# Performance work log

Measured on AMD Instinct MI355X. Metric: run time of the kernel, lower is better.

The kernel has to match this reference:

```python
import jax, jax.numpy as jnp
import numpy as np

DIM = 2048
DIM_HEAD = 128
HEADS = 16
BATCH = 1
SEQ = 2048
EPS = 1e-5
MASK_VALUE = 1e-10  # faithful to original module (not -inf)
SCALE = DIM_HEAD ** -0.5


def setup_inputs() -> dict:
    key = jax.random.key(0)
    ks = jax.random.split(key, 7)
    x = jax.random.normal(ks[0], (BATCH, SEQ, DIM), dtype=jnp.float32)
    pos_bias = jax.random.normal(ks[1], (HEADS, SEQ, SEQ), dtype=jnp.float32)
    gamma = jnp.ones((DIM,), dtype=jnp.float32)
    wq = jax.random.normal(ks[2], (DIM, HEADS * DIM_HEAD), dtype=jnp.float32)
    wk = jax.random.normal(ks[3], (DIM, DIM_HEAD), dtype=jnp.float32)
    wv = jax.random.normal(ks[4], (DIM, DIM_HEAD), dtype=jnp.float32)
    wo = jax.random.normal(ks[5], (HEADS * DIM_HEAD, DIM), dtype=jnp.float32)
    # causal mask [SEQ, SEQ]
    mask = jnp.tril(jnp.ones((SEQ, SEQ), dtype=jnp.bool_))
    return {"x": x, "pos_bias": pos_bias, "gamma": gamma,
            "wq": wq, "wk": wk, "wv": wv, "wo": wo, "mask": mask}


def reference(x, pos_bias, gamma, wq, wk, wv, wo, mask):
    # RMSNorm
    inv_norm = jax.lax.rsqrt(jnp.mean(jnp.square(x), axis=-1, keepdims=True) + EPS)
    xn = inv_norm * x * gamma
    # projections (multi-query: single shared K/V head)
    q = xn @ wq                                  # [b, n, h*d]
    k = xn @ wk                                  # [b, n, d]
    v = xn @ wv                                  # [b, n, d]
    b, n, _ = q.shape
    q = q.reshape(b, n, HEADS, DIM_HEAD).transpose(0, 2, 1, 3)  # [b, h, n, d]
    q = q * SCALE
    sim = jnp.einsum('bhid,bjd->bhij', q, k)     # [b, h, i, j]
    sim = sim + pos_bias                          # pos_bias [h, n, n] broadcasts
    sim = jnp.where(mask, sim, MASK_VALUE)
    attn = jax.nn.softmax(sim, axis=-1)
    out = jnp.einsum('bhij,bjd->bhid', attn, v)  # [b, h, n, d]
    out = out.transpose(0, 2, 1, 3).reshape(b, n, HEADS * DIM_HEAD)
    return out @ wo
```

## Files before the change

### kernel.cpp

```cpp
#include <hip/hip_runtime.h>
#include <math.h>

#define SEQ 2048
#define DIM 2048
#define NH 16
#define DH 128
#define NKV 2304
#define KOFF 2048
#define VOFF 2176
#define QK_SCALE 0.08838834764831845f

typedef _Float16 f16;
typedef _Float16 f16x8 __attribute__((ext_vector_type(8)));
typedef _Float16 f16x4 __attribute__((ext_vector_type(4)));
typedef float f32x4 __attribute__((ext_vector_type(4)));

__global__ __launch_bounds__(256) void rmsnorm_split_k(
    const float* __restrict__ x, const float* __restrict__ gamma,
    f16* __restrict__ oh, f16* __restrict__ ol)
{
    int row = blockIdx.x, tid = threadIdx.x;
    const float4* xr = (const float4*)(x + (size_t)row * DIM);
    float4 a0 = xr[tid], a1 = xr[tid + 256];
    float ss = a0.x*a0.x + a0.y*a0.y + a0.z*a0.z + a0.w*a0.w
             + a1.x*a1.x + a1.y*a1.y + a1.z*a1.z + a1.w*a1.w;
    #pragma unroll
    for (int off = 1; off < 64; off <<= 1) ss += __shfl_xor(ss, off, 64);
    __shared__ float red[4];
    if ((tid & 63) == 0) red[tid >> 6] = ss;
    __syncthreads();
    float inv = 1.0f / sqrtf((red[0] + red[1] + red[2] + red[3]) * (1.0f / DIM) + 1e-5f);
    const float4* gr = (const float4*)gamma;
    float4 g0 = gr[tid], g1 = gr[tid + 256];
    float v[8] = { a0.x*inv*g0.x, a0.y*inv*g0.y, a0.z*inv*g0.z, a0.w*inv*g0.w,
                   a1.x*inv*g1.x, a1.y*inv*g1.y, a1.z*inv*g1.z, a1.w*inv*g1.w };
    f16x4 h0, l0, h1, l1;
    #pragma unroll
    for (int i = 0; i < 4; i++) {
        f16 h = (f16)v[i];   h0[i] = h; l0[i] = (f16)(v[i]   - (float)h);
        f16 g = (f16)v[i+4]; h1[i] = g; l1[i] = (f16)(v[i+4] - (float)g);
    }
    size_t base = (size_t)row * DIM + tid * 4;
    *(f16x4*)&oh[base] = h0;  *(f16x4*)&oh[base + 1024] = h1;
    *(f16x4*)&ol[base] = l0;  *(f16x4*)&ol[base + 1024] = l1;
}

template<bool WLO>
__global__ __launch_bounds__(256) void transpose_split_k(
    const float* __restrict__ in, f16* __restrict__ oh, f16* __restrict__ ol,
    int ldin, int outld)
{
    __shared__ float t[32][33];
    int tx = threadIdx.x, ty = threadIdx.y;
    int c0 = blockIdx.x * 32, r0 = blockIdx.y * 32;
    #pragma unroll
    for (int yy = 0; yy < 4; yy++)
        t[ty + yy*8][tx] = in[(size_t)(r0 + ty + yy*8) * ldin + c0 + tx];
    __syncthreads();
    #pragma unroll
    for (int yy = 0; yy < 4; yy++) {
        float v = t[tx][ty + yy*8];
        size_t o = (size_t)(c0 + ty + yy*8) * outld + r0 + tx;
        f16 h = (f16)v; oh[o] = h;
        if (WLO) ol[o] = (f16)(v - (float)h);
    }
}

__global__ __launch_bounds__(256) void transpose_f16_k(
    const f16* __restrict__ in, f16* __restrict__ out, int ldin, int outld)
{
    __shared__ f16 t[32][33];
    int tx = threadIdx.x, ty = threadIdx.y;
    int c0 = blockIdx.x * 32, r0 = blockIdx.y * 32;
    #pragma unroll
    for (int yy = 0; yy < 4; yy++)
        t[ty + yy*8][tx] = in[(size_t)(r0 + ty + yy*8) * ldin + c0 + tx];
    __syncthreads();
    #pragma unroll
    for (int yy = 0; yy < 4; yy++)
        out[(size_t)(c0 + ty + yy*8) * outld + r0 + tx] = t[tx][ty + yy*8];
}

template<int PASSES, int OUTMODE>
__global__ __launch_bounds__(256) void gemm_k(
    const f16* __restrict__ Ah, const f16* __restrict__ Al,
    const f16* __restrict__ Bh, const f16* __restrict__ Bl,
    float* __restrict__ C, f16* __restrict__ Ch, f16* __restrict__ Cl,
    int N, int K, float scale, int scale_cols)
{
    __shared__ f16 sa_h[128][40];
    __shared__ f16 sb_h[128][40];
    __shared__ f16 sa_l[PASSES == 3 ? 128 : 1][40];
    __shared__ f16 sb_l[PASSES == 3 ? 128 : 1][40];
    int tid = threadIdx.x;
    int wave = tid >> 6, lane = tid & 63, quad = lane >> 4, l16 = lane & 15;
    int m0 = blockIdx.x * 128, n0 = blockIdx.y * 128;
    int wm = (wave & 1) * 64, wn = (wave >> 1) * 64;
    int srow = tid >> 2, sch = (tid & 3) * 8;
    f32x4 acc[4][4] = {};
    const f16* pa0 = Ah + (size_t)(m0 + srow) * K + sch;
    const f16* pa1 = Ah + (size_t)(m0 + srow + 64) * K + sch;
    const f16* pb0 = Bh + (size_t)(n0 + srow) * K + sch;
    const f16* pb1 = Bh + (size_t)(n0 + srow + 64) * K + sch;
    const f16* qa0 = Al + (size_t)(m0 + srow) * K + sch;
    const f16* qa1 = Al + (size_t)(m0 + srow + 64) * K + sch;
    const f16* qb0 = Bl + (size_t)(n0 + srow) * K + sch;
    const f16* qb1 = Bl + (size_t)(n0 + srow + 64) * K + sch;

    for (int k0 = 0; k0 < K; k0 += 32) {
        __syncthreads();
        *(f16x8*)&sa_h[srow][sch]      = *(const f16x8*)(pa0 + k0);
        *(f16x8*)&sa_h[srow + 64][sch] = *(const f16x8*)(pa1 + k0);
        *(f16x8*)&sb_h[srow][sch]      = *(const f16x8*)(pb0 + k0);
        *(f16x8*)&sb_h[srow + 64][sch] = *(const f16x8*)(pb1 + k0);
        if constexpr (PASSES == 3) {
            *(f16x8*)&sa_l[srow][sch]      = *(const f16x8*)(qa0 + k0);
            *(f16x8*)&sa_l[srow + 64][sch] = *(const f16x8*)(qa1 + k0);
            *(f16x8*)&sb_l[srow][sch]      = *(const f16x8*)(qb0 + k0);
            *(f16x8*)&sb_l[srow + 64][sch] = *(const f16x8*)(qb1 + k0);
        }
        __syncthreads();
        f16x8 ah[4], bh[4], al[4], bl[4];
        #pragma unroll
        for (int t = 0; t < 4; t++) {
            ah[t] = *(const f16x8*)&sa_h[wm + t*16 + l16][quad * 8];
            bh[t] = *(const f16x8*)&sb_h[wn + t*16 + l16][quad * 8];
        }
        if constexpr (PASSES == 3) {
            #pragma unroll
            for (int t = 0; t < 4; t++) {
                al[t] = *(const f16x8*)&sa_l[wm + t*16 + l16][quad * 8];
                bl[t] = *(const f16x8*)&sb_l[wn + t*16 + l16][quad * 8];
            }
        }
        #pragma unroll
        for (int i = 0; i < 4; i++)
            #pragma unroll
            for (int j = 0; j < 4; j++) {
                acc[i][j] = __builtin_amdgcn_mfma_f32_16x16x32_f16(ah[i], bh[j], acc[i][j], 0, 0, 0);
                if constexpr (PASSES == 3) {
                    acc[i][j] = __builtin_amdgcn_mfma_f32_16x16x32_f16(ah[i], bl[j], acc[i][j], 0, 0, 0);
                    acc[i][j] = __builtin_amdgcn_mfma_f32_16x16x32_f16(al[i], bh[j], acc[i][j], 0, 0, 0);
                }
            }
    }
    #pragma unroll
    for (int i = 0; i < 4; i++)
        #pragma unroll
        for (int j = 0; j < 4; j++) {
            int row = m0 + wm + i*16 + quad*4;
            int col = n0 + wn + j*16 + l16;
            float s = (col < scale_cols) ? scale : 1.0f;
            #pragma unroll
            for (int r = 0; r < 4; r++) {
                float v = acc[i][j][r] * s;
                if constexpr (OUTMODE == 0) {
                    C[(size_t)(row + r) * N + col] = v;
                } else {
                    f16 h = (f16)v;
                    Ch[(size_t)(row + r) * N + col] = h;
                    Cl[(size_t)(row + r) * N + col] = (f16)(v - (float)h);
                }
            }
        }
}

__global__ __launch_bounds__(256) void attn_k(
    const f16* __restrict__ Ph, const f16* __restrict__ Pl,
    const f16* __restrict__ Vt, const float* __restrict__ bias,
    f16* __restrict__ Out)
{
    __shared__ f16 skh[64][136];
    __shared__ f16 skl[64][136];
    __shared__ f16 sv[128][72];
    __shared__ f16 sp[4][16][72];
    int tid = threadIdx.x, wave = tid >> 6, lane = tid & 63;
    int quad = lane >> 4, l16 = lane & 15;
    int h = blockIdx.y;
    int i0 = blockIdx.x * 64;
    int qrow = i0 + wave * 16 + l16;

    f16x8 qh[4], ql[4];
    #pragma unroll
    for (int kt = 0; kt < 4; kt++) {
        size_t off = (size_t)qrow * NKV + h * DH + kt * 32 + quad * 8;
        qh[kt] = *(const f16x8*)(Ph + off);
        ql[kt] = *(const f16x8*)(Pl + off);
    }
    f32x4 o[8];
    f32x4 zero = {0.f, 0.f, 0.f, 0.f};
    #pragma unroll
    for (int dt = 0; dt < 8; dt++) o[dt] = zero;
    float mrun[4], lrun[4];
    #pragma unroll
    for (int r = 0; r < 4; r++) { mrun[r] = -1e30f; lrun[r] = 0.f; }

    int krow = tid >> 2, kc4 = tid & 3;
    int vd = tid >> 1, vcg = tid & 1;
    const float* brow = bias + (size_t)h * SEQ * SEQ;
    int ibase = i0 + wave * 16 + quad * 4;

    for (int j0 = 0; j0 < SEQ; j0 += 64) {
        __syncthreads();
        #pragma unroll
        for (int cc = 0; cc < 4; cc++) {
            int ch = kc4 + cc * 4;
            size_t goff = (size_t)(j0 + krow) * NKV + KOFF + ch * 8;
            *(f16x8*)&skh[krow][ch * 8] = *(const f16x8*)(Ph + goff);
            *(f16x8*)&skl[krow][ch * 8] = *(const f16x8*)(Pl + goff);
        }
        #pragma unroll
        for (int cc = 0; cc < 4; cc++) {
            int ch = vcg + cc * 2;
            *(f16x8*)&sv[vd][ch * 8] = *(const f16x8*)(Vt + (size_t)vd * SEQ + j0 + ch * 8);
        }
        __syncthreads();

        f32x4 s[4];
        #pragma unroll
        for (int nt = 0; nt < 4; nt++) s[nt] = zero;
        #pragma unroll
        for (int nt = 0; nt < 4; nt++)
            #pragma unroll
            for (int kt = 0; kt < 4; kt++) {
                f16x8 kh = *(const f16x8*)&skh[nt*16 + l16][kt*32 + quad*8];
                f16x8 kl = *(const f16x8*)&skl[nt*16 + l16][kt*32 + quad*8];
                s[nt] = __builtin_amdgcn_mfma_f32_16x16x32_f16(qh[kt], kh, s[nt], 0, 0, 0);
                s[nt] = __builtin_amdgcn_mfma_f32_16x16x32_f16(qh[kt], kl, s[nt], 0, 0, 0);
                s[nt] = __builtin_amdgcn_mfma_f32_16x16x32_f16(ql[kt], kh, s[nt], 0, 0, 0);
            }
        #pragma unroll
        for (int nt = 0; nt < 4; nt++) {
            int jg = j0 + nt*16 + l16;
            #pragma unroll
            for (int r = 0; r < 4; r++) {
                int ig = ibase + r;
                float v = s[nt][r] + brow[(size_t)ig * SEQ + jg];
                s[nt][r] = (jg <= ig) ? v : 1e-10f;
            }
        }
        #pragma unroll
        for (int r = 0; r < 4; r++) {
            float mx = fmaxf(fmaxf(s[0][r], s[1][r]), fmaxf(s[2][r], s[3][r]));
            mx = fmaxf(mx, __shfl_xor(mx, 1, 64));
            mx = fmaxf(mx, __shfl_xor(mx, 2, 64));
            mx = fmaxf(mx, __shfl_xor(mx, 4, 64));
            mx = fmaxf(mx, __shfl_xor(mx, 8, 64));
            float mn = fmaxf(mrun[r], mx);
            float alpha = __expf(mrun[r] - mn);
            mrun[r] = mn;
            float rs = 0.f;
            #pragma unroll
            for (int nt = 0; nt < 4; nt++) {
                float p = __expf(s[nt][r] - mn);
                s[nt][r] = p; rs += p;
            }
            rs += __shfl_xor(rs, 1, 64);
            rs += __shfl_xor(rs, 2, 64);
            rs += __shfl_xor(rs, 4, 64);
            rs += __shfl_xor(rs, 8, 64);
            lrun[r] = lrun[r] * alpha + rs;
            #pragma unroll
            for (int dt = 0; dt < 8; dt++) o[dt][r] *= alpha;
            #pragma unroll
            for (int nt = 0; nt < 4; nt++)
                sp[wave][quad*4 + r][nt*16 + l16] = (f16)s[nt][r];
        }
        #pragma unroll
        for (int ks = 0; ks < 2; ks++) {
            f16x8 pa = *(const f16x8*)&sp[wave][l16][ks*32 + quad*8];
            #pragma unroll
            for (int dt = 0; dt < 8; dt++) {
                f16x8 vb = *(const f16x8*)&sv[dt*16 + l16][ks*32 + quad*8];
                o[dt] = __builtin_amdgcn_mfma_f32_16x16x32_f16(pa, vb, o[dt], 0, 0, 0);
            }
        }
    }
    #pragma unroll
    for (int dt = 0; dt < 8; dt++) {
        int col = h * DH + dt*16 + l16;
        #pragma unroll
        for (int r = 0; r < 4; r++) {
            int ig = i0 + wave*16 + quad*4 + r;
            Out[(size_t)ig * DIM + col] = (f16)(o[dt][r] / lrun[r]);
        }
    }
}

extern "C" void kernel_launch(void* const* d_in, const int* in_sizes, int n_in,
                              void* d_out, int out_size, void* d_ws, size_t ws_size,
                              hipStream_t stream)
{
    const float* x     = (const float*)d_in[0];
    const float* bias  = (const float*)d_in[1];
    const float* gamma = (const float*)d_in[2];
    const float* wq    = (const float*)d_in[3];
    const float* wk    = (const float*)d_in[4];
    const float* wv    = (const float*)d_in[5];
    const float* wo    = (const float*)d_in[6];
    float* out = (float*)d_out;
    char* ws = (char*)d_ws;

    const size_t MB = 1024 * 1024;
    f16* xn_h   = (f16*)(ws);
    f16* xn_l   = (f16*)(ws + 8  * MB);
    f16* wT_h   = (f16*)(ws + 16 * MB);
    f16* wT_l   = (f16*)(ws + 25 * MB);
    f16* woT_h  = (f16*)(ws + 34 * MB);
    f16* proj_h = (f16*)(ws + 42 * MB);
    f16* proj_l = (f16*)(ws + 51 * MB);
    f16* attn_o = xn_h;
    f16* vT     = xn_l;

    dim3 tb(32, 8);

    rmsnorm_split_k<<<SEQ, 256, 0, stream>>>(x, gamma, xn_h, xn_l);

    transpose_split_k<true><<<dim3(64, 64), tb, 0, stream>>>(wq, wT_h, wT_l, DIM, DIM);
    transpose_split_k<true><<<dim3(4, 64),  tb, 0, stream>>>(wk, wT_h + (size_t)KOFF * DIM,
                                                             wT_l + (size_t)KOFF * DIM, DH, DIM);
    transpose_split_k<true><<<dim3(4, 64),  tb, 0, stream>>>(wv, wT_h + (size_t)VOFF * DIM,
                                                             wT_l + (size_t)VOFF * DIM, DH, DIM);
    transpose_split_k<false><<<dim3(64, 64), tb, 0, stream>>>(wo, woT_h, nullptr, DIM, DIM);

    gemm_k<3, 1><<<dim3(16, 18), 256, 0, stream>>>(xn_h, xn_l, wT_h, wT_l,
                                                   nullptr, proj_h, proj_l,
                                                   NKV, DIM, QK_SCALE, DIM);

    transpose_f16_k<<<dim3(4, 64), tb, 0, stream>>>(proj_h + VOFF, vT, NKV, SEQ);

    attn_k<<<dim3(32, 16), 256, 0, stream>>>(proj_h, proj_l, vT, bias, attn_o);

    gemm_k<1, 0><<<dim3(16, 16), 256, 0, stream>>>(attn_o, attn_o, woT_h, woT_h,
                                                   out, nullptr, nullptr,
                                                   DIM, DIM, 1.0f, 0);
}
```

Before: 642.7 us.

## Skip masked attention tiles via closed-form suffix sum; use direct global-to-LDS loads in GEMM

The attention kernel now iterates only over key tiles up to the causal diagonal. A precomputed suffix sum of V accounts in closed form for the masked positions, which carry the constant logit 1e-10, so their contribution is folded into the final softmax normalization exactly. Query blocks are launched in reverse order so the longest blocks start first. The GEMM replaces register-staged shared-memory stores with global_load_lds into unpadded tiles, which may add LDS bank conflicts in exchange for lower register and VALU cost.

```diff
diff --git a/kernel.cpp b/kernel.cpp
--- a/kernel.cpp
+++ b/kernel.cpp
@@ -14,6 +14,13 @@
 typedef _Float16 f16x8 __attribute__((ext_vector_type(8)));
 typedef _Float16 f16x4 __attribute__((ext_vector_type(4)));
 typedef float f32x4 __attribute__((ext_vector_type(4)));
+
+__device__ __forceinline__ void gload16(const f16* g, f16* l) {
+    __builtin_amdgcn_global_load_lds(
+        (const __attribute__((address_space(1))) void*)g,
+        (__attribute__((address_space(3))) void*)l,
+        16, 0, 0);
+}
 
 __global__ __launch_bounds__(256) void rmsnorm_split_k(
     const float* __restrict__ x, const float* __restrict__ gamma,
@@ -81,6 +88,28 @@
         out[(size_t)(c0 + ty + yy*8) * outld + r0 + tx] = t[tx][ty + yy*8];
 }
 
+__global__ __launch_bounds__(64) void vsuf_k(
+    const f16* __restrict__ Vt, float* __restrict__ Vsuf)
+{
+    int d = blockIdx.x;
+    int lane = threadIdx.x;
+    float vals[32]; float s = 0.f;
+    const f16* row = Vt + (size_t)d * SEQ + lane * 32;
+    #pragma unroll
+    for (int u = 0; u < 32; u++) { vals[u] = (float)row[u]; s += vals[u]; }
+    float acc = s;
+    #pragma unroll
+    for (int off = 1; off < 64; off <<= 1) {
+        float other = __shfl_down(acc, off, 64);
+        if (lane + off < 64) acc += other;
+    }
+    float run = acc - s;
+    for (int u = 31; u >= 0; u--) {
+        Vsuf[(size_t)(lane * 32 + u) * DH + d] = run;
+        run += vals[u];
+    }
+}
+
 template<int PASSES, int OUTMODE>
 __global__ __launch_bounds__(256) void gemm_k(
     const f16* __restrict__ Ah, const f16* __restrict__ Al,
@@ -88,49 +117,59 @@
     float* __restrict__ C, f16* __restrict__ Ch, f16* __restrict__ Cl,
     int N, int K, float scale, int scale_cols)
 {
-    __shared__ f16 sa_h[128][40];
-    __shared__ f16 sb_h[128][40];
-    __shared__ f16 sa_l[PASSES == 3 ? 128 : 1][40];
-    __shared__ f16 sb_l[PASSES == 3 ? 128 : 1][40];
+    __shared__ f16 sa_h[128 * 32];
+    __shared__ f16 sb_h[128 * 32];
+    __shared__ f16 sa_l[PASSES == 3 ? 128 * 32 : 8];
+    __shared__ f16 sb_l[PASSES == 3 ? 128 * 32 : 8];
     int tid = threadIdx.x;
     int wave = tid >> 6, lane = tid & 63, quad = lane >> 4, l16 = lane & 15;
     int m0 = blockIdx.x * 128, n0 = blockIdx.y * 128;
     int wm = (wave & 1) * 64, wn = (wave >> 1) * 64;
-    int srow = tid >> 2, sch = (tid & 3) * 8;
     f32x4 acc[4][4] = {};
-    const f16* pa0 = Ah + (size_t)(m0 + srow) * K + sch;
-    const f16* pa1 = Ah + (size_t)(m0 + srow + 64) * K + sch;
-    const f16* pb0 = Bh + (size_t)(n0 + srow) * K + sch;
-    const f16* pb1 = Bh + (size_t)(n0 + srow + 64) * K + sch;
-    const f16* qa0 = Al + (size_t)(m0 + srow) * K + sch;
-    const f16* qa1 = Al + (size_t)(m0 + srow + 64) * K + sch;
-    const f16* qb0 = Bl + (size_t)(n0 + srow) * K + sch;
-    const f16* qb1 = Bl + (size_t)(n0 + srow + 64) * K + sch;
+
+    int r0s = wave * 16 + (lane >> 2);
+    int cs  = (lane & 3) * 8;
+    const f16* gA0 = Ah + (size_t)(m0 + r0s) * K + cs;
+    const f16* gA1 = Ah + (size_t)(m0 + r0s + 64) * K + cs;
+    const f16* gB0 = Bh + (size_t)(n0 + r0s) * K + cs;
+    const f16* gB1 = Bh + (size_t)(n0 + r0s + 64) * K + cs;
+    const f16* hA0 = Al + (size_t)(m0 + r0s) * K + cs;
+    const f16* hA1 = Al + (size_t)(m0 + r0s + 64) * K + cs;
+    const f16* hB0 = Bl + (size_t)(n0 + r0s) * K + cs;
+    const f16* hB1 = Bl + (size_t)(n0 + r0s + 64) * K + cs;
+    f16* lA0 = &sa_h[(size_t)r0s * 32 + cs];
+    f16* lA1 = &sa_h[(size_t)(r0s + 64) * 32 + cs];
+    f16* lB0 = &sb_h[(size_t)r0s * 32 + cs];
+    f16* lB1 = &sb_h[(size_t)(r0s + 64) * 32 + cs];
+    f16* mA0 = &sa_l[(size_t)r0s * 32 + cs];
+    f16* mA1 = &sa_l[(size_t)(r0s + 64) * 32 + cs];
+    f16* mB0 = &sb_l[(size_t)r0s * 32 + cs];
+    f16* mB1 = &sb_l[(size_t)(r0s + 64) * 32 + cs];
 
     for (int k0 = 0; k0 < K; k0 += 32) {
         __syncthreads();
-        *(f16x8*)&sa_h[srow][sch]      = *(const f16x8*)(pa0 + k0);
-        *(f16x8*)&sa_h[srow + 64][sch] = *(const f16x8*)(pa1 + k0);
-        *(f16x8*)&sb_h[srow][sch]      = *(const f16x8*)(pb0 + k0);
-        *(f16x8*)&sb_h[srow + 64][sch] = *(const f16x8*)(pb1 + k0);
+        gload16(gA0 + k0, lA0);
+        gload16(gA1 + k0, lA1);
+        gload16(gB0 + k0, lB0);
+        gload16(gB1 + k0, lB1);
         if constexpr (PASSES == 3) {
-            *(f16x8*)&sa_l[srow][sch]      = *(const f16x8*)(qa0 + k0);
-            *(f16x8*)&sa_l[srow + 64][sch] = *(const f16x8*)(qa1 + k0);
-            *(f16x8*)&sb_l[srow][sch]      = *(const f16x8*)(qb0 + k0);
-            *(f16x8*)&sb_l[srow + 64][sch] = *(const f16x8*)(qb1 + k0);
+            gload16(hA0 + k0, mA0);
+            gload16(hA1 + k0, mA1);
+            gload16(hB0 + k0, mB0);
+            gload16(hB1 + k0, mB1);
         }
         __syncthreads();
         f16x8 ah[4], bh[4], al[4], bl[4];
         #pragma unroll
         for (int t = 0; t < 4; t++) {
-            ah[t] = *(const f16x8*)&sa_h[wm + t*16 + l16][quad * 8];
-            bh[t] = *(const f16x8*)&sb_h[wn + t*16 + l16][quad * 8];
+            ah[t] = *(const f16x8*)&sa_h[(wm + t*16 + l16) * 32 + quad * 8];
+            bh[t] = *(const f16x8*)&sb_h[(wn + t*16 + l16) * 32 + quad * 8];
         }
         if constexpr (PASSES == 3) {
             #pragma unroll
             for (int t = 0; t < 4; t++) {
-                al[t] = *(const f16x8*)&sa_l[wm + t*16 + l16][quad * 8];
-                bl[t] = *(const f16x8*)&sb_l[wn + t*16 + l16][quad * 8];
+                al[t] = *(const f16x8*)&sa_l[(wm + t*16 + l16) * 32 + quad * 8];
+                bl[t] = *(const f16x8*)&sb_l[(wn + t*16 + l16) * 32 + quad * 8];
             }
         }
         #pragma unroll
@@ -168,7 +207,7 @@
 __global__ __launch_bounds__(256) void attn_k(
     const f16* __restrict__ Ph, const f16* __restrict__ Pl,
     const f16* __restrict__ Vt, const float* __restrict__ bias,
-    f16* __restrict__ Out)
+    const float* __restrict__ Vsuf, f16* __restrict__ Out)
 {
     __shared__ f16 skh[64][136];
     __shared__ f16 skl[64][136];
@@ -177,7 +216,7 @@
     int tid = threadIdx.x, wave = tid >> 6, lane = tid & 63;
     int quad = lane >> 4, l16 = lane & 15;
     int h = blockIdx.y;
-    int i0 = blockIdx.x * 64;
+    int i0 = ((int)gridDim.x - 1 - (int)blockIdx.x) * 64;
     int qrow = i0 + wave * 16 + l16;
 
     f16x8 qh[4], ql[4];
@@ -200,7 +239,9 @@
     const float* brow = bias + (size_t)h * SEQ * SEQ;
     int ibase = i0 + wave * 16 + quad * 4;
 
-    for (int j0 = 0; j0 < SEQ; j0 += 64) {
+    int ntile = i0 / 64 + 1;
+    for (int jt = 0; jt < ntile; jt++) {
+        int j0 = jt * 64;
         __syncthreads();
         #pragma unroll
         for (int cc = 0; cc < 4; cc++) {
@@ -282,7 +323,13 @@
         #pragma unroll
         for (int r = 0; r < 4; r++) {
             int ig = i0 + wave*16 + quad*4 + r;
-            Out[(size_t)ig * DIM + col] = (f16)(o[dt][r] / lrun[r]);
+            int nmask = SEQ - 1 - ig;
+            float mfin = fmaxf(mrun[r], 1e-10f);
+            float al = __expf(mrun[r] - mfin);
+            float pm = (nmask > 0) ? __expf(1e-10f - mfin) : 0.f;
+            float lfin = lrun[r] * al + (float)nmask * pm;
+            float num = o[dt][r] * al + pm * Vsuf[(size_t)ig * DH + dt*16 + l16];
+            Out[(size_t)ig * DIM + col] = (f16)(num / lfin);
         }
     }
 }
@@ -309,6 +356,7 @@
     f16* woT_h  = (f16*)(ws + 34 * MB);
     f16* proj_h = (f16*)(ws + 42 * MB);
     f16* proj_l = (f16*)(ws + 51 * MB);
+    float* vsuf = (float*)(ws + 60 * MB);
     f16* attn_o = xn_h;
     f16* vT     = xn_l;
 
@@ -328,8 +376,9 @@
                                                    NKV, DIM, QK_SCALE, DIM);
 
     transpose_f16_k<<<dim3(4, 64), tb, 0, stream>>>(proj_h + VOFF, vT, NKV, SEQ);
-
-    attn_k<<<dim3(32, 16), 256, 0, stream>>>(proj_h, proj_l, vT, bias, attn_o);
+    vsuf_k<<<DH, 64, 0, stream>>>(vT, vsuf);
+
+    attn_k<<<dim3(32, 16), 256, 0, stream>>>(proj_h, proj_l, vT, bias, vsuf, attn_o);
 
     gemm_k<1, 0><<<dim3(16, 16), 256, 0, stream>>>(attn_o, attn_o, woT_h, woT_h,
                                                    out, nullptr, nullptr,
```

Measured after the change: 783.1 us. +21.8%, slower.
